# Optimization experiments

Hardware: AMD Instinct MI355X
Metric: run time of the kernel (lower is better)

## Reference

```python
import jax, jax.numpy as jnp
import numpy as np

N = 100000
IN_C = 256
OUT_C = 256
E = 500000


def gcn_conv(x, W, b, edges):
    """PyG GCNConv: add self-loops, symmetric D^-1/2 (A+I) D^-1/2 normalization,
    then scatter-add of transformed source features into targets, plus bias."""
    n = x.shape[0]
    loop = jnp.arange(n, dtype=edges.dtype)
    row = jnp.concatenate([edges[0], loop])  # source
    col = jnp.concatenate([edges[1], loop])  # target
    deg = jax.ops.segment_sum(jnp.ones_like(col, dtype=x.dtype), col, num_segments=n)
    dis = jax.lax.rsqrt(deg)  # deg >= 1 after self-loops
    norm = dis[row] * dis[col]  # [E+n]
    h = x @ W  # [n, out]
    msg = h[row] * norm[:, None]  # gather + scale
    return jax.ops.segment_sum(msg, col, num_segments=n) + b


def setup_inputs() -> dict:
    key = jax.random.key(0)
    ks = jax.random.split(key, 24)
    x = jax.random.normal(ks[0], (N, IN_C), dtype=jnp.float32)
    edges00 = jax.random.randint(ks[1], (2, E), 0, N, dtype=jnp.int32)
    edges01 = jax.random.randint(ks[2], (2, E), 0, N, dtype=jnp.int32)
    edges10 = jax.random.randint(ks[3], (2, E), 0, N, dtype=jnp.int32)
    edges11 = jax.random.randint(ks[4], (2, E), 0, N, dtype=jnp.int32)
    t0 = (jax.random.uniform(ks[5], (N,)) > 0.5).astype(jnp.float32)
    t1 = 1.0 - t0
    scale = 1.0 / np.sqrt(IN_C)
    W1 = jax.random.normal(ks[6], (IN_C, OUT_C), dtype=jnp.float32) * scale
    W2 = jax.random.normal(ks[7], (IN_C, OUT_C), dtype=jnp.float32) * scale
    W3 = jax.random.normal(ks[8], (IN_C, OUT_C), dtype=jnp.float32) * scale
    W4 = jax.random.normal(ks[9], (IN_C, OUT_C), dtype=jnp.float32) * scale
    b1 = jnp.zeros((OUT_C,), jnp.float32)
    b2 = jnp.zeros((OUT_C,), jnp.float32)
    b3 = jnp.zeros((OUT_C,), jnp.float32)
    b4 = jnp.zeros((OUT_C,), jnp.float32)
    p0 = jax.random.normal(ks[10], (OUT_C,), dtype=jnp.float32)
    p1 = jax.random.normal(ks[11], (OUT_C,), dtype=jnp.float32)
    p2 = jax.random.normal(ks[12], (OUT_C,), dtype=jnp.float32)
    p3 = jax.random.normal(ks[13], (OUT_C,), dtype=jnp.float32)
    p4 = jax.random.normal(ks[14], (OUT_C,), dtype=jnp.float32)
    p5 = jax.random.normal(ks[15], (OUT_C,), dtype=jnp.float32)
    return dict(x=x, edges00=edges00, edges01=edges01, edges10=edges10, edges11=edges11,
                type0_idx=t0, type1_idx=t1,
                W1=W1, b1=b1, W2=W2, b2=b2, W3=W3, b3=b3, W4=W4, b4=b4,
                p0=p0, p1=p1, p2=p2, p3=p3, p4=p4, p5=p5)


def reference(x, edges00, edges01, edges10, edges11, type0_idx, type1_idx,
              W1, b1, W2, b2, W3, b3, W4, b4, p0, p1, p2, p3, p4, p5):
    # x0/x1: first feature column masked by node type, broadcast over out channels
    x0c = type0_idx * x[:, 0]  # [N]
    x1c = type1_idx * x[:, 0]
    x00 = gcn_conv(x, W1, b1, edges00)
    x01 = gcn_conv(x, W2, b2, edges01)
    x10 = gcn_conv(x, W3, b3, edges10)
    x11 = gcn_conv(x, W4, b4, edges11)
    out = (x0c[:, None] * p0 + x1c[:, None] * p1
           + x00 * p2 + x01 * p3 + x10 * p4 + x11 * p5)
    return out
```

## Files before the change

### kernel.cpp

```cpp
#include <hip/hip_runtime.h>


#define PCAP 24

typedef __bf16 v8bf __attribute__((ext_vector_type(8)));
typedef float v4f __attribute__((ext_vector_type(4)));

__device__ __forceinline__ unsigned short f2bf(float f) {
  unsigned u = __float_as_uint(f);
  u += 0x7fffu + ((u >> 16) & 1u);
  return (unsigned short)(u >> 16);
}
__device__ __forceinline__ float bf2f(unsigned short s) {
  return __uint_as_float(((unsigned)s) << 16);
}
__device__ __forceinline__ void async_ld16(const void* g, void* l) {
  __builtin_amdgcn_global_load_lds((__attribute__((address_space(1))) void*)g,
                                   (__attribute__((address_space(3))) void*)l,
                                   16, 0, 0);
}

__global__ void lc_zero(int* __restrict__ p, int n) {
  int i = blockIdx.x * 256 + threadIdx.x;
  if (i < n) p[i] = 0;
}

__global__ void lc_fill(const int* __restrict__ e0, const int* __restrict__ e1,
                        const int* __restrict__ e2, const int* __restrict__ e3,
                        int* __restrict__ cursor, int* __restrict__ payload,
                        int N, int E) {
  int e = blockIdx.x * 256 + threadIdx.x;
  if (e >= E) return;
  int k = blockIdx.y;
  const int* ed = (k == 0) ? e0 : (k == 1) ? e1 : (k == 2) ? e2 : e3;
  int src = ed[e], col = ed[E + e];
  int idx = k * N + col;
  int pos = atomicAdd(&cursor[idx], 1);
  if (pos < PCAP) payload[idx * PCAP + pos] = src;
}

__global__ void lc_dis(const int* __restrict__ deg, float* __restrict__ dis, int M) {
  int i = blockIdx.x * 256 + threadIdx.x;
  if (i < M) dis[i] = rsqrtf((float)(deg[i] + 1));
}

__global__ void lc_bias(const float* __restrict__ b1, const float* __restrict__ b2,
                        const float* __restrict__ b3, const float* __restrict__ b4,
                        const float* __restrict__ p2, const float* __restrict__ p3,
                        const float* __restrict__ p4, const float* __restrict__ p5,
                        float* __restrict__ biasc) {
  int c = threadIdx.x;
  biasc[c] = b1[c] * p2[c] + b2[c] * p3[c] + b3[c] * p4[c] + b4[c] * p5[c];
}

__global__ void lc_prep(const float* __restrict__ W1, const float* __restrict__ W2,
                        const float* __restrict__ W3, const float* __restrict__ W4,
                        const float* __restrict__ p2, const float* __restrict__ p3,
                        const float* __restrict__ p4, const float* __restrict__ p5,
                        unsigned short* __restrict__ Wt) {
  int b = blockIdx.x;
  int k = b >> 8, co = b & 255;
  int kk = threadIdx.x;
  const float* W = (k == 0) ? W1 : (k == 1) ? W2 : (k == 2) ? W3 : W4;
  const float* p = (k == 0) ? p2 : (k == 1) ? p3 : (k == 2) ? p4 : p5;
  Wt[(size_t)co * 1024 + k * 256 + kk] = f2bf(W[kk * 256 + co] * p[co]);
}

__global__ void lc_cvt(const float4* __restrict__ x4, ushort4* __restrict__ xb4,
                       const float* __restrict__ t0, const float* __restrict__ t1,
                       float* __restrict__ m0, float* __restrict__ m1, int n4) {
  int i = blockIdx.x * 256 + threadIdx.x;
  if (i >= n4) return;
  float4 v = x4[i];
  ushort4 r;
  r.x = f2bf(v.x); r.y = f2bf(v.y); r.z = f2bf(v.z); r.w = f2bf(v.w);
  xb4[i] = r;
  if ((i & 63) == 0) {
    int n = i >> 6;
    float xc = v.x;
    m0[n] = t0[n] * xc;
    m1[n] = t1[n] * xc;
  }
}

__global__ __launch_bounds__(256) void lc_aggx(
    const unsigned short* __restrict__ xb, unsigned short* __restrict__ Agg,
    int aggw, int kcount, int kbase, const int* __restrict__ deg,
    const float* __restrict__ dis, const int* __restrict__ payload, int N) {
  int t = threadIdx.x;
  int w = t >> 6, lane = t & 63;
  int n, k, koff;
  if (kcount == 4) { n = blockIdx.x; k = w; koff = k * 256; }
  else { n = blockIdx.x * 4 + w; k = kbase; koff = 0; }
  if (n >= N) return;
  int c = lane * 4;
  int idx = k * N + n;
  int kN = k * N;

  float dn = dis[idx];
  float s = dn * dn;
  ushort4 hv = *(const ushort4*)&xb[(size_t)n * 256 + c];
  float a0 = bf2f(hv.x) * s, a1 = bf2f(hv.y) * s;
  float a2 = bf2f(hv.z) * s, a3 = bf2f(hv.w) * s;

  int start = idx * PCAP;
  int cnt = deg[idx];
  if (cnt > PCAP) cnt = PCAP;
  int i = 0;
  for (; i + 4 <= cnt; i += 4) {
    int s0 = payload[start + i];
    int s1 = payload[start + i + 1];
    int s2 = payload[start + i + 2];
    int s3 = payload[start + i + 3];
    ushort4 g0 = *(const ushort4*)&xb[(size_t)s0 * 256 + c];
    ushort4 g1 = *(const ushort4*)&xb[(size_t)s1 * 256 + c];
    ushort4 g2 = *(const ushort4*)&xb[(size_t)s2 * 256 + c];
    ushort4 g3 = *(const ushort4*)&xb[(size_t)s3 * 256 + c];
    float n0 = dis[kN + s0] * dn, n1 = dis[kN + s1] * dn;
    float n2 = dis[kN + s2] * dn, n3 = dis[kN + s3] * dn;
    a0 += bf2f(g0.x) * n0 + bf2f(g1.x) * n1 + bf2f(g2.x) * n2 + bf2f(g3.x) * n3;
    a1 += bf2f(g0.y) * n0 + bf2f(g1.y) * n1 + bf2f(g2.y) * n2 + bf2f(g3.y) * n3;
    a2 += bf2f(g0.z) * n0 + bf2f(g1.z) * n1 + bf2f(g2.z) * n2 + bf2f(g3.z) * n3;
    a3 += bf2f(g0.w) * n0 + bf2f(g1.w) * n1 + bf2f(g2.w) * n2 + bf2f(g3.w) * n3;
  }
  for (; i < cnt; i++) {
    int s0 = payload[start + i];
    ushort4 g0 = *(const ushort4*)&xb[(size_t)s0 * 256 + c];
    float n0 = dis[kN + s0] * dn;
    a0 += bf2f(g0.x) * n0;
    a1 += bf2f(g0.y) * n0;
    a2 += bf2f(g0.z) * n0;
    a3 += bf2f(g0.w) * n0;
  }
  ushort4 r;
  r.x = f2bf(a0); r.y = f2bf(a1); r.z = f2bf(a2); r.w = f2bf(a3);
  *(ushort4*)&Agg[(size_t)n * aggw + koff + c] = r;
}

__global__ __launch_bounds__(512, 4) void lc_gemm(
    const unsigned short* __restrict__ A, int strideA,
    const unsigned short* __restrict__ B, int strideB, int K,
    float* __restrict__ out, int Mrows, int addprev, int doepi,
    const float* __restrict__ m0, const float* __restrict__ m1,
    const float* __restrict__ p0, const float* __restrict__ p1,
    const float* __restrict__ biasc) {
  __shared__ alignas(16) unsigned short As[128 * 32];
  __shared__ alignas(16) unsigned short Bs[256 * 32];
  int t = threadIdx.x;
  int w = t >> 6, lane = t & 63;
  int wm = w & 1, wn = w >> 1;
  int quad = lane >> 4, l16 = lane & 15;
  int row0 = blockIdx.x * 128;

  v4f acc[4][4];
#pragma unroll
  for (int mt = 0; mt < 4; mt++)
#pragma unroll
    for (int nt = 0; nt < 4; nt++) {
      v4f z = {0.f, 0.f, 0.f, 0.f};
      acc[mt][nt] = z;
    }

  const int ra = t >> 2;
  const int e0 = (t & 3) * 8;
  const int sws = (ra & 3) << 3;
  const unsigned swf = (unsigned)((l16 & 3) << 3);

  for (int kk = 0; kk < K; kk += 32) {
    {
      int grow = row0 + ra;
      if (grow >= Mrows) grow = Mrows - 1;
      async_ld16(A + (size_t)grow * strideA + kk + (e0 ^ sws), &As[ra * 32 + e0]);
      async_ld16(B + (size_t)ra * strideB + kk + (e0 ^ sws), &Bs[ra * 32 + e0]);
      async_ld16(B + (size_t)(128 + ra) * strideB + kk + (e0 ^ sws),
                 &Bs[(128 + ra) * 32 + e0]);
    }
    __syncthreads();

    v8bf af[4], bfr[4];
    unsigned eq = ((unsigned)(quad * 8)) ^ swf;
#pragma unroll
    for (int mt = 0; mt < 4; mt++) {
      int r = wm * 64 + mt * 16 + l16;
      af[mt] = *(const v8bf*)&As[(unsigned)r * 32 + eq];
    }
#pragma unroll
    for (int nt = 0; nt < 4; nt++) {
      int n = wn * 64 + nt * 16 + l16;
      bfr[nt] = *(const v8bf*)&Bs[(unsigned)n * 32 + eq];
    }
#pragma unroll
    for (int mt = 0; mt < 4; mt++)
#pragma unroll
      for (int nt = 0; nt < 4; nt++)
        acc[mt][nt] =
            __builtin_amdgcn_mfma_f32_16x16x32_bf16(af[mt], bfr[nt], acc[mt][nt], 0, 0, 0);
    __syncthreads();
  }

  float pc0[4], pc1[4], bc[4];
#pragma unroll
  for (int nt = 0; nt < 4; nt++) {
    int gcol = wn * 64 + nt * 16 + l16;
    pc0[nt] = doepi ? p0[gcol] : 0.f;
    pc1[nt] = doepi ? p1[gcol] : 0.f;
    bc[nt] = doepi ? biasc[gcol] : 0.f;
  }
#pragma unroll
  for (int mt = 0; mt < 4; mt++)
#pragma unroll
    for (int r = 0; r < 4; r++) {
      int grow = row0 + wm * 64 + mt * 16 + quad * 4 + r;
      if (grow >= Mrows) continue;
      float m0v = 0.f, m1v = 0.f;
      if (doepi) { m0v = m0[grow]; m1v = m1[grow]; }
#pragma unroll
      for (int nt = 0; nt < 4; nt++) {
        int gcol = wn * 64 + nt * 16 + l16;
        size_t o = (size_t)grow * 256 + gcol;
        float v = acc[mt][nt][r];
        if (addprev) v += out[o];
        if (doepi) v += m0v * pc0[nt] + m1v * pc1[nt] + bc[nt];
        out[o] = v;
      }
    }
}

extern "C" void kernel_launch(void* const* d_in, const int* in_sizes, int n_in,
                              void* d_out, int out_size, void* d_ws, size_t ws_size,
                              hipStream_t stream) {
  const float* x = (const float*)d_in[0];
  const int* e00 = (const int*)d_in[1];
  const int* e01 = (const int*)d_in[2];
  const int* e10 = (const int*)d_in[3];
  const int* e11 = (const int*)d_in[4];
  const float* t0 = (const float*)d_in[5];
  const float* t1 = (const float*)d_in[6];
  const float* W1 = (const float*)d_in[7];
  const float* b1 = (const float*)d_in[8];
  const float* W2 = (const float*)d_in[9];
  const float* b2 = (const float*)d_in[10];
  const float* W3 = (const float*)d_in[11];
  const float* b3 = (const float*)d_in[12];
  const float* W4 = (const float*)d_in[13];
  const float* b4 = (const float*)d_in[14];
  const float* p0 = (const float*)d_in[15];
  const float* p1 = (const float*)d_in[16];
  const float* p2 = (const float*)d_in[17];
  const float* p3 = (const float*)d_in[18];
  const float* p4 = (const float*)d_in[19];
  const float* p5 = (const float*)d_in[20];
  float* out = (float*)d_out;

  int N = in_sizes[0] / 256;
  int E = in_sizes[1] / 2;
  int M4 = 4 * N;

  char* wp = (char*)d_ws;
  auto carve = [&](size_t bytes) {
    void* r = (void*)wp;
    wp += (bytes + 255) & ~(size_t)255;
    return r;
  };
  unsigned short* xb = (unsigned short*)carve((size_t)N * 256 * 2);
  unsigned short* Wt = (unsigned short*)carve((size_t)256 * 1024 * 2);
  int* cursor = (int*)carve((size_t)M4 * 4);
  float* dis = (float*)carve((size_t)M4 * 4);
  float* biasc = (float*)carve(256 * 4);
  float* m0 = (float*)carve((size_t)N * 4);
  float* m1 = (float*)carve((size_t)N * 4);
  int* payload = (int*)carve((size_t)M4 * PCAP * 4);
  size_t used = (size_t)(wp - (char*)d_ws);
  size_t remain = (ws_size > used) ? ws_size - used : 0;
  bool fat = remain >= (size_t)N * 1024 * 2;
  unsigned short* Agg = (unsigned short*)wp;

  int gE = (E + 255) / 256;
  int gM = (M4 + 255) / 256;

  lc_zero<<<gM, 256, 0, stream>>>(cursor, M4);
  lc_fill<<<dim3(gE, 4), 256, 0, stream>>>(e00, e01, e10, e11, cursor, payload, N, E);
  lc_dis<<<gM, 256, 0, stream>>>(cursor, dis, M4);
  lc_bias<<<1, 256, 0, stream>>>(b1, b2, b3, b4, p2, p3, p4, p5, biasc);
  lc_prep<<<1024, 256, 0, stream>>>(W1, W2, W3, W4, p2, p3, p4, p5, Wt);
  lc_cvt<<<(N * 64 + 255) / 256, 256, 0, stream>>>((const float4*)x, (ushort4*)xb,
                                                   t0, t1, m0, m1, N * 64);

  int gemm_mb = (N + 127) / 128;
  if (fat) {
    lc_aggx<<<N, 256, 0, stream>>>(xb, Agg, 1024, 4, 0, cursor, dis, payload, N);
    lc_gemm<<<gemm_mb, 512, 0, stream>>>(Agg, 1024, Wt, 1024, 1024, out, N,
                                         0, 1, m0, m1, p0, p1, biasc);
  } else {
    for (int k = 0; k < 4; k++) {
      lc_aggx<<<(N + 3) / 4, 256, 0, stream>>>(xb, Agg, 256, 1, k, cursor, dis,
                                               payload, N);
      lc_gemm<<<gemm_mb, 512, 0, stream>>>(Agg, 256, Wt + k * 256, 1024, 256,
                                           out, N, (k > 0) ? 1 : 0,
                                           (k == 3) ? 1 : 0, m0, m1, p0, p1,
                                           biasc);
    }
  }
}
```

Before: 706.1 us.

## Pack quantized source normalization into edge payload, merge bias into prep kernel

A new lc_pack pass stores each neighbour's source D^-1/2 factor, quantized to 15 bits, in the upper bits of its payload word; the low 17 bits keep the source index. The aggregation kernel then decodes the weight straight from the payload instead of doing a second dependent gather into dis. The intent is to shorten the latency chain and cut random loads in the gather-heavy aggregation, at the cost of an extra pass over the payload and a small precision loss in the normalization. The 17-bit index field assumes N stays at or below 131072. The bias computation is folded into lc_prep to save a launch, and the GEMM launch bound drops its min-blocks hint, which may change register allocation.

```diff
diff --git a/kernel.cpp b/kernel.cpp
--- a/kernel.cpp
+++ b/kernel.cpp
@@ -27,7 +27,7 @@
 
 __global__ void lc_fill(const int* __restrict__ e0, const int* __restrict__ e1,
                         const int* __restrict__ e2, const int* __restrict__ e3,
-                        int* __restrict__ cursor, int* __restrict__ payload,
+                        int* __restrict__ cursor, unsigned* __restrict__ payload,
                         int N, int E) {
   int e = blockIdx.x * 256 + threadIdx.x;
   if (e >= E) return;
@@ -36,7 +36,7 @@
   int src = ed[e], col = ed[E + e];
   int idx = k * N + col;
   int pos = atomicAdd(&cursor[idx], 1);
-  if (pos < PCAP) payload[idx * PCAP + pos] = src;
+  if (pos < PCAP) payload[(size_t)idx * PCAP + pos] = (unsigned)src;
 }
 
 __global__ void lc_dis(const int* __restrict__ deg, float* __restrict__ dis, int M) {
@@ -44,26 +44,40 @@
   if (i < M) dis[i] = rsqrtf((float)(deg[i] + 1));
 }
 
-__global__ void lc_bias(const float* __restrict__ b1, const float* __restrict__ b2,
+__global__ void lc_pack(unsigned* __restrict__ payload, const int* __restrict__ deg,
+                        const float* __restrict__ dis, int N) {
+  int i = blockIdx.x * 256 + threadIdx.x;
+  if (i >= N * PCAP) return;
+  int k = blockIdx.y;
+  int col = i / PCAP, slot = i - col * PCAP;
+  int list = k * N + col;
+  int cnt = deg[list];
+  if (cnt > PCAP) cnt = PCAP;
+  if (slot >= cnt) return;
+  size_t pidx = (size_t)list * PCAP + slot;
+  unsigned src = payload[pidx];
+  float ds = dis[(size_t)k * N + src];
+  unsigned q = (unsigned)(ds * 32767.0f + 0.5f);
+  payload[pidx] = (q << 17) | src;
+}
+
+__global__ void lc_prep(const float* __restrict__ W1, const float* __restrict__ W2,
+                        const float* __restrict__ W3, const float* __restrict__ W4,
+                        const float* __restrict__ b1, const float* __restrict__ b2,
                         const float* __restrict__ b3, const float* __restrict__ b4,
                         const float* __restrict__ p2, const float* __restrict__ p3,
                         const float* __restrict__ p4, const float* __restrict__ p5,
-                        float* __restrict__ biasc) {
-  int c = threadIdx.x;
-  biasc[c] = b1[c] * p2[c] + b2[c] * p3[c] + b3[c] * p4[c] + b4[c] * p5[c];
-}
-
-__global__ void lc_prep(const float* __restrict__ W1, const float* __restrict__ W2,
-                        const float* __restrict__ W3, const float* __restrict__ W4,
-                        const float* __restrict__ p2, const float* __restrict__ p3,
-                        const float* __restrict__ p4, const float* __restrict__ p5,
-                        unsigned short* __restrict__ Wt) {
+                        unsigned short* __restrict__ Wt, float* __restrict__ biasc) {
   int b = blockIdx.x;
   int k = b >> 8, co = b & 255;
   int kk = threadIdx.x;
   const float* W = (k == 0) ? W1 : (k == 1) ? W2 : (k == 2) ? W3 : W4;
   const float* p = (k == 0) ? p2 : (k == 1) ? p3 : (k == 2) ? p4 : p5;
   Wt[(size_t)co * 1024 + k * 256 + kk] = f2bf(W[kk * 256 + co] * p[co]);
+  if (b == 0) {
+    int c = kk;
+    biasc[c] = b1[c] * p2[c] + b2[c] * p3[c] + b3[c] * p4[c] + b4[c] * p5[c];
+  }
 }
 
 __global__ void lc_cvt(const float4* __restrict__ x4, ushort4* __restrict__ xb4,
@@ -86,7 +100,7 @@
 __global__ __launch_bounds__(256) void lc_aggx(
     const unsigned short* __restrict__ xb, unsigned short* __restrict__ Agg,
     int aggw, int kcount, int kbase, const int* __restrict__ deg,
-    const float* __restrict__ dis, const int* __restrict__ payload, int N) {
+    const float* __restrict__ dis, const unsigned* __restrict__ payload, int N) {
   int t = threadIdx.x;
   int w = t >> 6, lane = t & 63;
   int n, k, koff;
@@ -95,38 +109,41 @@
   if (n >= N) return;
   int c = lane * 4;
   int idx = k * N + n;
-  int kN = k * N;
 
   float dn = dis[idx];
+  float dns = dn * (1.0f / 32767.0f);
   float s = dn * dn;
   ushort4 hv = *(const ushort4*)&xb[(size_t)n * 256 + c];
   float a0 = bf2f(hv.x) * s, a1 = bf2f(hv.y) * s;
   float a2 = bf2f(hv.z) * s, a3 = bf2f(hv.w) * s;
 
-  int start = idx * PCAP;
+  size_t start = (size_t)idx * PCAP;
   int cnt = deg[idx];
   if (cnt > PCAP) cnt = PCAP;
   int i = 0;
   for (; i + 4 <= cnt; i += 4) {
-    int s0 = payload[start + i];
-    int s1 = payload[start + i + 1];
-    int s2 = payload[start + i + 2];
-    int s3 = payload[start + i + 3];
+    unsigned p0v = payload[start + i];
+    unsigned p1v = payload[start + i + 1];
+    unsigned p2v = payload[start + i + 2];
+    unsigned p3v = payload[start + i + 3];
+    unsigned s0 = p0v & 0x1FFFFu, s1 = p1v & 0x1FFFFu;
+    unsigned s2 = p2v & 0x1FFFFu, s3 = p3v & 0x1FFFFu;
     ushort4 g0 = *(const ushort4*)&xb[(size_t)s0 * 256 + c];
     ushort4 g1 = *(const ushort4*)&xb[(size_t)s1 * 256 + c];
     ushort4 g2 = *(const ushort4*)&xb[(size_t)s2 * 256 + c];
     ushort4 g3 = *(const ushort4*)&xb[(size_t)s3 * 256 + c];
-    float n0 = dis[kN + s0] * dn, n1 = dis[kN + s1] * dn;
-    float n2 = dis[kN + s2] * dn, n3 = dis[kN + s3] * dn;
+    float n0 = (float)(p0v >> 17) * dns, n1 = (float)(p1v >> 17) * dns;
+    float n2 = (float)(p2v >> 17) * dns, n3 = (float)(p3v >> 17) * dns;
     a0 += bf2f(g0.x) * n0 + bf2f(g1.x) * n1 + bf2f(g2.x) * n2 + bf2f(g3.x) * n3;
     a1 += bf2f(g0.y) * n0 + bf2f(g1.y) * n1 + bf2f(g2.y) * n2 + bf2f(g3.y) * n3;
     a2 += bf2f(g0.z) * n0 + bf2f(g1.z) * n1 + bf2f(g2.z) * n2 + bf2f(g3.z) * n3;
     a3 += bf2f(g0.w) * n0 + bf2f(g1.w) * n1 + bf2f(g2.w) * n2 + bf2f(g3.w) * n3;
   }
   for (; i < cnt; i++) {
-    int s0 = payload[start + i];
+    unsigned p0v = payload[start + i];
+    unsigned s0 = p0v & 0x1FFFFu;
     ushort4 g0 = *(const ushort4*)&xb[(size_t)s0 * 256 + c];
-    float n0 = dis[kN + s0] * dn;
+    float n0 = (float)(p0v >> 17) * dns;
     a0 += bf2f(g0.x) * n0;
     a1 += bf2f(g0.y) * n0;
     a2 += bf2f(g0.z) * n0;
@@ -137,7 +154,7 @@
   *(ushort4*)&Agg[(size_t)n * aggw + koff + c] = r;
 }
 
-__global__ __launch_bounds__(512, 4) void lc_gemm(
+__global__ __launch_bounds__(512) void lc_gemm(
     const unsigned short* __restrict__ A, int strideA,
     const unsigned short* __restrict__ B, int strideB, int K,
     float* __restrict__ out, int Mrows, int addprev, int doepi,
@@ -269,7 +286,7 @@
   float* biasc = (float*)carve(256 * 4);
   float* m0 = (float*)carve((size_t)N * 4);
   float* m1 = (float*)carve((size_t)N * 4);
-  int* payload = (int*)carve((size_t)M4 * PCAP * 4);
+  unsigned* payload = (unsigned*)carve((size_t)M4 * PCAP * 4);
   size_t used = (size_t)(wp - (char*)d_ws);
   size_t remain = (ws_size > used) ? ws_size - used : 0;
   bool fat = remain >= (size_t)N * 1024 * 2;
@@ -277,12 +294,14 @@
 
   int gE = (E + 255) / 256;
   int gM = (M4 + 255) / 256;
+  int gP = (N * PCAP + 255) / 256;
 
   lc_zero<<<gM, 256, 0, stream>>>(cursor, M4);
   lc_fill<<<dim3(gE, 4), 256, 0, stream>>>(e00, e01, e10, e11, cursor, payload, N, E);
   lc_dis<<<gM, 256, 0, stream>>>(cursor, dis, M4);
-  lc_bias<<<1, 256, 0, stream>>>(b1, b2, b3, b4, p2, p3, p4, p5, biasc);
-  lc_prep<<<1024, 256, 0, stream>>>(W1, W2, W3, W4, p2, p3, p4, p5, Wt);
+  lc_pack<<<dim3(gP, 4), 256, 0, stream>>>(payload, cursor, dis, N);
+  lc_prep<<<1024, 256, 0, stream>>>(W1, W2, W3, W4, b1, b2, b3, b4,
+                                    p2, p3, p4, p5, Wt, biasc);
   lc_cvt<<<(N * 64 + 255) / 256, 256, 0, stream>>>((const float4*)x, (ushort4*)xb,
                                                    t0, t1, m0, m1, N * 64);
 
```

New measurement: 707.3 us. Within noise of the previous version (+0.2%).
